# Optimization experiments

Hardware: AMD Instinct MI355X
Metric: run time of the kernel (lower is better)

Reference implementation:

```python
import jax, jax.numpy as jnp
import numpy as np

THRESHOLD = 0.5


def setup_inputs() -> dict:
    key = jax.random.key(0)
    k1, k2 = jax.random.split(key)
    L, C, H, W = 5, 256, 128, 256
    node_feature = jax.random.normal(k1, (L, C, H, W), dtype=jnp.float32)
    mlp_w = jax.random.normal(k2, (1, C), dtype=jnp.float32) * (1.0 / np.sqrt(C))
    mlp_b = jnp.zeros((1,), dtype=jnp.float32)
    return {"node_feature": node_feature, "mlp_w": mlp_w, "mlp_b": mlp_b}


def reference(node_feature, mlp_w, mlp_b):
    L, C, H, W = node_feature.shape
    HW = H * W
    # rearrange 'l c h w -> (h w) l c'
    x = node_feature.reshape(L, C, HW).transpose(2, 0, 1)  # (HW, L, C)
    ego = x[:, :1, :]                                       # (HW, 1, C)
    nbr = x[:, 1:, :]                                       # (HW, L-1, C)
    # per-pixel attention: query = ego broadcast over L-1 slots
    q = jnp.broadcast_to(ego, (HW, L - 1, C))
    score = jnp.einsum('nqc,nkc->nqk', q, nbr) / np.float32(np.sqrt(C))  # (HW, L-1, L-1)
    attn = jax.nn.softmax(score, axis=-1)
    context = jnp.einsum('nqk,nkc->nqc', attn, nbr)         # (HW, L-1, C)
    # linear -> relu -> sigmoid gate
    gate = jax.nn.sigmoid(jax.nn.relu(context @ mlp_w.T + mlp_b))  # (HW, L-1, 1)
    # dilate_kernel == 1 path: hard threshold mask
    mask = (gate > THRESHOLD).astype(x.dtype)               # (HW, L-1, 1)
    ego_mask = jnp.ones((HW, 1, 1), dtype=x.dtype)
    overall_mask = jnp.concatenate([ego_mask, mask], axis=1)  # (HW, L, 1)
    x = x * overall_mask
    # rearrange '(h w) l c -> l c h w'
    return x.transpose(1, 2, 0).reshape(L, C, H, W)
```

## Files before the change

kernel.cpp:

```cpp
#include <hip/hip_runtime.h>
#include <math.h>

#define HW_SZ 32768
#define C_SZ  256
#define L_SZ  5
#define CHW   (C_SZ * HW_SZ)

typedef float vfloat4 __attribute__((ext_vector_type(4)));

__global__ __launch_bounds__(1024, 1) void is_fused_kernel(
    const float* __restrict__ x,
    const float* __restrict__ mlp_w,
    const float* __restrict__ mlp_b,
    float* __restrict__ out)
{
    __shared__ float w_sh[C_SZ];
    __shared__ float part[16][16][8][5];
    __shared__ float m_sh[64];

    const int tid  = threadIdx.x;
    const int wv   = tid >> 6;
    const int lane = tid & 63;
    const int ci4  = lane >> 4;
    const int ni16 = lane & 15;
    const int n0   = blockIdx.x * 64 + ni16 * 4;

    if (tid < C_SZ) w_sh[tid] = mlp_w[tid];
    __syncthreads();

    const int cb = 16 * wv + ci4;
    const float* bp = x   + cb * HW_SZ + n0;
    float*       op = out + cb * HW_SZ + n0;

    vfloat4 v[5][4];
    #pragma unroll
    for (int l = 0; l < 5; ++l)
        #pragma unroll
        for (int j = 0; j < 4; ++j)
            v[l][j] = *(const vfloat4*)(bp + l * CHW + j * 4 * HW_SZ);

    vfloat4 s[4] = {{0,0,0,0},{0,0,0,0},{0,0,0,0},{0,0,0,0}};
    vfloat4 t[4] = {{0,0,0,0},{0,0,0,0},{0,0,0,0},{0,0,0,0}};
    #pragma unroll
    for (int j = 0; j < 4; ++j) {
        const float wc = w_sh[cb + 4 * j];
        #pragma unroll
        for (int k = 0; k < 4; ++k) {
            s[k] += v[0][j] * v[k + 1][j];
            t[k] += wc      * v[k + 1][j];
        }
    }

    #pragma unroll
    for (int j = 0; j < 4; ++j)
        __builtin_nontemporal_store(v[0][j], (vfloat4*)(op + j * 4 * HW_SZ));

    #pragma unroll
    for (int m = 16; m <= 32; m <<= 1) {
        #pragma unroll
        for (int k = 0; k < 4; ++k) {
            #pragma unroll
            for (int c = 0; c < 4; ++c) {
                s[k][c] += __shfl_xor(s[k][c], m, 64);
                t[k][c] += __shfl_xor(t[k][c], m, 64);
            }
        }
    }
    if (ci4 == 0) {
        #pragma unroll
        for (int k = 0; k < 4; ++k)
            #pragma unroll
            for (int c = 0; c < 4; ++c) {
                part[wv][ni16][k][c]     = s[k][c];
                part[wv][ni16][k + 4][c] = t[k][c];
            }
    }
    __syncthreads();

    if (tid < 64) {
        const int g = tid >> 2, cc = tid & 3;
        float ss[4] = {0, 0, 0, 0}, tt[4] = {0, 0, 0, 0};
        #pragma unroll
        for (int w8 = 0; w8 < 16; ++w8) {
            #pragma unroll
            for (int k = 0; k < 4; ++k) {
                ss[k] += part[w8][g][k][cc];
                tt[k] += part[w8][g][k + 4][cc];
            }
        }
        const float scale = 0.0625f;
        #pragma unroll
        for (int k = 0; k < 4; ++k) ss[k] *= scale;

        const float smax = fmaxf(fmaxf(ss[0], ss[1]), fmaxf(ss[2], ss[3]));
        const float p0 = expf(ss[0] - smax);
        const float p1 = expf(ss[1] - smax);
        const float p2 = expf(ss[2] - smax);
        const float p3 = expf(ss[3] - smax);
        const float z  = (p0 * tt[0] + p1 * tt[1] + p2 * tt[2] + p3 * tt[3])
                         / ((p0 + p1) + (p2 + p3)) + mlp_b[0];
        m_sh[tid] = (z > 0.f) ? 1.f : 0.f;
    }
    __syncthreads();

    const int nl = ni16 * 4;
    vfloat4 m4;
    m4.x = m_sh[nl];     m4.y = m_sh[nl + 1];
    m4.z = m_sh[nl + 2]; m4.w = m_sh[nl + 3];

    #pragma unroll
    for (int l = 1; l < 5; ++l)
        #pragma unroll
        for (int j = 0; j < 4; ++j)
            __builtin_nontemporal_store(v[l][j] * m4,
                                        (vfloat4*)(op + l * CHW + j * 4 * HW_SZ));
}

extern "C" void kernel_launch(void* const* d_in, const int* in_sizes, int n_in,
                              void* d_out, int out_size, void* d_ws, size_t ws_size,
                              hipStream_t stream) {
    const float* x = (const float*)d_in[0];
    const float* w = (const float*)d_in[1];
    const float* b = (const float*)d_in[2];
    float* out = (float*)d_out;

    hipLaunchKernelGGL(is_fused_kernel, dim3(HW_SZ / 64), dim3(1024), 0, stream,
                       x, w, b, out);
}
```

Before: 65.44 us.

## Process two pixel tiles per block and use LDS-only barriers

Each block now loops over two 64-pixel tiles, halving the grid to 256 blocks and hoisting the weight and bias loads out of the per-tile work. It also replaces __syncthreads with a custom barrier that waits only on LDS counters, so outstanding global stores need not drain before each barrier. The cost is that the loop with unroll 1 serialises loads across tiles with no prefetch, and an extra barrier per iteration. Fewer blocks may leave some of the GPU's compute units underused.

```diff
diff --git a/kernel.cpp b/kernel.cpp
--- a/kernel.cpp
+++ b/kernel.cpp
@@ -7,6 +7,14 @@
 #define CHW   (C_SZ * HW_SZ)
 
 typedef float vfloat4 __attribute__((ext_vector_type(4)));
+
+
+__device__ __forceinline__ void sync_lds_only() {
+    asm volatile("s_waitcnt lgkmcnt(0)" ::: "memory");
+    __builtin_amdgcn_sched_barrier(0);
+    __builtin_amdgcn_s_barrier();
+    __builtin_amdgcn_sched_barrier(0);
+}
 
 __global__ __launch_bounds__(1024, 1) void is_fused_kernel(
     const float* __restrict__ x,
@@ -23,97 +31,106 @@
     const int lane = tid & 63;
     const int ci4  = lane >> 4;
     const int ni16 = lane & 15;
-    const int n0   = blockIdx.x * 64 + ni16 * 4;
 
     if (tid < C_SZ) w_sh[tid] = mlp_w[tid];
-    __syncthreads();
+    sync_lds_only();
 
     const int cb = 16 * wv + ci4;
-    const float* bp = x   + cb * HW_SZ + n0;
-    float*       op = out + cb * HW_SZ + n0;
+    const float bias = mlp_b[0];
+    float wcs[4];
+    #pragma unroll
+    for (int j = 0; j < 4; ++j) wcs[j] = w_sh[cb + 4 * j];
 
-    vfloat4 v[5][4];
-    #pragma unroll
-    for (int l = 0; l < 5; ++l)
+    #pragma unroll 1
+    for (int t = 0; t < 2; ++t) {
+        const int n0 = (blockIdx.x * 2 + t) * 64 + ni16 * 4;
+        const float* bp = x   + cb * HW_SZ + n0;
+        float*       op = out + cb * HW_SZ + n0;
+
+        vfloat4 v[5][4];
+        #pragma unroll
+        for (int l = 0; l < 5; ++l)
+            #pragma unroll
+            for (int j = 0; j < 4; ++j)
+                v[l][j] = *(const vfloat4*)(bp + l * CHW + j * 4 * HW_SZ);
+
+        vfloat4 s[4] = {{0,0,0,0},{0,0,0,0},{0,0,0,0},{0,0,0,0}};
+        vfloat4 tt4[4] = {{0,0,0,0},{0,0,0,0},{0,0,0,0},{0,0,0,0}};
+        #pragma unroll
+        for (int j = 0; j < 4; ++j) {
+            #pragma unroll
+            for (int k = 0; k < 4; ++k) {
+                s[k]   += v[0][j] * v[k + 1][j];
+                tt4[k] += wcs[j]  * v[k + 1][j];
+            }
+        }
+
         #pragma unroll
         for (int j = 0; j < 4; ++j)
-            v[l][j] = *(const vfloat4*)(bp + l * CHW + j * 4 * HW_SZ);
+            __builtin_nontemporal_store(v[0][j], (vfloat4*)(op + j * 4 * HW_SZ));
 
-    vfloat4 s[4] = {{0,0,0,0},{0,0,0,0},{0,0,0,0},{0,0,0,0}};
-    vfloat4 t[4] = {{0,0,0,0},{0,0,0,0},{0,0,0,0},{0,0,0,0}};
-    #pragma unroll
-    for (int j = 0; j < 4; ++j) {
-        const float wc = w_sh[cb + 4 * j];
         #pragma unroll
-        for (int k = 0; k < 4; ++k) {
-            s[k] += v[0][j] * v[k + 1][j];
-            t[k] += wc      * v[k + 1][j];
-        }
-    }
-
-    #pragma unroll
-    for (int j = 0; j < 4; ++j)
-        __builtin_nontemporal_store(v[0][j], (vfloat4*)(op + j * 4 * HW_SZ));
-
-    #pragma unroll
-    for (int m = 16; m <= 32; m <<= 1) {
-        #pragma unroll
-        for (int k = 0; k < 4; ++k) {
+        for (int m = 16; m <= 32; m <<= 1) {
             #pragma unroll
-            for (int c = 0; c < 4; ++c) {
-                s[k][c] += __shfl_xor(s[k][c], m, 64);
-                t[k][c] += __shfl_xor(t[k][c], m, 64);
+            for (int k = 0; k < 4; ++k) {
+                #pragma unroll
+                for (int c = 0; c < 4; ++c) {
+                    s[k][c]   += __shfl_xor(s[k][c], m, 64);
+                    tt4[k][c] += __shfl_xor(tt4[k][c], m, 64);
+                }
             }
         }
+        if (ci4 == 0) {
+            #pragma unroll
+            for (int k = 0; k < 4; ++k)
+                #pragma unroll
+                for (int c = 0; c < 4; ++c) {
+                    part[wv][ni16][k][c]     = s[k][c];
+                    part[wv][ni16][k + 4][c] = tt4[k][c];
+                }
+        }
+        sync_lds_only();
+
+        if (tid < 64) {
+            const int g = tid >> 2, cc = tid & 3;
+            float ss[4] = {0, 0, 0, 0}, tz[4] = {0, 0, 0, 0};
+            #pragma unroll
+            for (int w8 = 0; w8 < 16; ++w8) {
+                #pragma unroll
+                for (int k = 0; k < 4; ++k) {
+                    ss[k] += part[w8][g][k][cc];
+                    tz[k] += part[w8][g][k + 4][cc];
+                }
+            }
+            const float scale = 0.0625f;
+            #pragma unroll
+            for (int k = 0; k < 4; ++k) ss[k] *= scale;
+
+            const float smax = fmaxf(fmaxf(ss[0], ss[1]), fmaxf(ss[2], ss[3]));
+            const float p0 = expf(ss[0] - smax);
+            const float p1 = expf(ss[1] - smax);
+            const float p2 = expf(ss[2] - smax);
+            const float p3 = expf(ss[3] - smax);
+            const float z  = (p0 * tz[0] + p1 * tz[1] + p2 * tz[2] + p3 * tz[3])
+                             / ((p0 + p1) + (p2 + p3)) + bias;
+            m_sh[tid] = (z > 0.f) ? 1.f : 0.f;
+        }
+        sync_lds_only();
+
+        const int nl = ni16 * 4;
+        vfloat4 m4;
+        m4.x = m_sh[nl];     m4.y = m_sh[nl + 1];
+        m4.z = m_sh[nl + 2]; m4.w = m_sh[nl + 3];
+
+        #pragma unroll
+        for (int l = 1; l < 5; ++l)
+            #pragma unroll
+            for (int j = 0; j < 4; ++j)
+                __builtin_nontemporal_store(v[l][j] * m4,
+                                            (vfloat4*)(op + l * CHW + j * 4 * HW_SZ));
+
+        sync_lds_only();
     }
-    if (ci4 == 0) {
-        #pragma unroll
-        for (int k = 0; k < 4; ++k)
-            #pragma unroll
-            for (int c = 0; c < 4; ++c) {
-                part[wv][ni16][k][c]     = s[k][c];
-                part[wv][ni16][k + 4][c] = t[k][c];
-            }
-    }
-    __syncthreads();
-
-    if (tid < 64) {
-        const int g = tid >> 2, cc = tid & 3;
-        float ss[4] = {0, 0, 0, 0}, tt[4] = {0, 0, 0, 0};
-        #pragma unroll
-        for (int w8 = 0; w8 < 16; ++w8) {
-            #pragma unroll
-            for (int k = 0; k < 4; ++k) {
-                ss[k] += part[w8][g][k][cc];
-                tt[k] += part[w8][g][k + 4][cc];
-            }
-        }
-        const float scale = 0.0625f;
-        #pragma unroll
-        for (int k = 0; k < 4; ++k) ss[k] *= scale;
-
-        const float smax = fmaxf(fmaxf(ss[0], ss[1]), fmaxf(ss[2], ss[3]));
-        const float p0 = expf(ss[0] - smax);
-        const float p1 = expf(ss[1] - smax);
-        const float p2 = expf(ss[2] - smax);
-        const float p3 = expf(ss[3] - smax);
-        const float z  = (p0 * tt[0] + p1 * tt[1] + p2 * tt[2] + p3 * tt[3])
-                         / ((p0 + p1) + (p2 + p3)) + mlp_b[0];
-        m_sh[tid] = (z > 0.f) ? 1.f : 0.f;
-    }
-    __syncthreads();
-
-    const int nl = ni16 * 4;
-    vfloat4 m4;
-    m4.x = m_sh[nl];     m4.y = m_sh[nl + 1];
-    m4.z = m_sh[nl + 2]; m4.w = m_sh[nl + 3];
-
-    #pragma unroll
-    for (int l = 1; l < 5; ++l)
-        #pragma unroll
-        for (int j = 0; j < 4; ++j)
-            __builtin_nontemporal_store(v[l][j] * m4,
-                                        (vfloat4*)(op + l * CHW + j * 4 * HW_SZ));
 }
 
 extern "C" void kernel_launch(void* const* d_in, const int* in_sizes, int n_in,
@@ -124,6 +141,6 @@
     const float* b = (const float*)d_in[2];
     float* out = (float*)d_out;
 
-    hipLaunchKernelGGL(is_fused_kernel, dim3(HW_SZ / 64), dim3(1024), 0, stream,
+    hipLaunchKernelGGL(is_fused_kernel, dim3(HW_SZ / 128), dim3(1024), 0, stream,
                        x, w, b, out);
 }
```

Measured after the change: 76.91 us. +17.5%, slower.
